# Performance work log

Hardware: AMD Instinct MI355X
Metric: run time of the kernel (lower is better)

Reference implementation:

```python
import jax, jax.numpy as jnp
import numpy as np

# --- CT geometry (stand-in for ctlib `options`): parallel-beam Radon transform ---
H = 256; W = 256          # image size
V = 192                   # number of projection views
D = 256                   # detector bins
S = 256                   # samples along each ray
_SQ2 = float(np.sqrt(2.0))
_ANG = jnp.asarray(np.linspace(0.0, np.pi, V, endpoint=False), jnp.float32)      # view angles
_DET = jnp.asarray(np.linspace(-_SQ2, _SQ2, D), jnp.float32)                      # detector coords (world units, image in [-1,1]^2)
_T   = jnp.asarray(np.linspace(-_SQ2, _SQ2, S), jnp.float32)                      # sample positions along ray
_DT  = jnp.float32(2.0 * _SQ2 / S)                                                # ray step length


def _bilerp(img, xp, yp):
    """Bilinear gather from img [H,W] at pixel coords xp,yp; zero outside."""
    x0 = jnp.floor(xp); y0 = jnp.floor(yp)
    ix0 = x0.astype(jnp.int32); iy0 = y0.astype(jnp.int32)
    fx = xp - x0; fy = yp - y0
    def gat(ix, iy):
        valid = (ix >= 0) & (ix < W) & (iy >= 0) & (iy < H)
        v = img[jnp.clip(iy, 0, H - 1), jnp.clip(ix, 0, W - 1)]
        return jnp.where(valid, v, jnp.float32(0.0))
    return (gat(ix0, iy0) * (1 - fx) * (1 - fy)
            + gat(ix0 + 1, iy0) * fx * (1 - fy)
            + gat(ix0, iy0 + 1) * (1 - fx) * fy
            + gat(ix0 + 1, iy0 + 1) * fx * fy)


def project2d(img):
    """Ray-driven forward projection: img [H,W] -> sinogram [V,D]."""
    cos = jnp.cos(_ANG)[:, None, None]; sin = jnp.sin(_ANG)[:, None, None]
    s = _DET[None, :, None]; t = _T[None, None, :]
    # world coords of sample points along each ray: [V,D,S]
    xw = -s * sin + t * cos
    yw = s * cos + t * sin
    # world [-1,1] -> pixel coords
    xp = (xw + 1.0) * (W / 2.0) - 0.5
    yp = (yw + 1.0) * (H / 2.0) - 0.5
    return _bilerp(img, xp, yp).sum(-1) * _DT


def backproject2d(sino):
    """Exact adjoint of project2d (ray-driven scatter): [V,D] -> [H,W]."""
    _, vjp_fn = jax.vjp(project2d, jnp.zeros((H, W), sino.dtype))
    return vjp_fn(sino)[0]


def setup_inputs() -> dict:
    key = jax.random.key(0)
    k1, k2, k3 = jax.random.split(key, 3)
    input_data = jax.random.normal(k1, (2, 1, H, W), jnp.float32)
    proj = jax.random.normal(k2, (2, 1, V, D), jnp.float32)
    weight = jax.random.uniform(k3, (1,), jnp.float32)
    return {"input_data": input_data, "proj": proj, "weight": weight}


def reference(input_data, proj, weight):
    B, C = input_data.shape[:2]
    imgs = input_data.reshape(B * C, H, W)
    sino = jax.vmap(project2d)(imgs).reshape(proj.shape)          # A x
    temp = sino - proj                                            # A x - p
    ir = jax.vmap(backproject2d)(temp.reshape(B * C, V, D)).reshape(input_data.shape)  # A^T (A x - p)
    return input_data - weight * ir
```

## Files before the change

### kernel.cpp

```cpp
#include <hip/hip_runtime.h>
#include <math.h>

#define HH 256
#define WW 256
#define VV 192
#define DD 256
#define SS 256

#define DSQ2      1.41421356237309504880
#define F_DT      ((float)(2.0 * DSQ2 / 256.0))
#define F_INV_DS  ((float)(255.0 / (2.0 * DSQ2)))
#define F_SIG     ((float)(256.0 * DSQ2 / 255.0))
#define F_RAD     ((float)(128.0 * DSQ2))

#define TPITCH 67
#define NSEG 8
#define NV (VV / NSEG)

static __device__ __forceinline__ float view_angle(int v) {
    return (float)((double)v * (3.14159265358979323846 / 192.0));
}

__global__ __launch_bounds__(256)
void fwd_tile_kernel(const float* __restrict__ img_all,
                     float* __restrict__ sacc) {
    __shared__ float tile[66 * TPITCH];
    __shared__ float red[4][64];
    const int tx = (blockIdx.x & 3) << 6;
    const int ty = (blockIdx.x >> 2) << 6;
    const int v  = blockIdx.y;
    const int b  = blockIdx.z;
    const int tid  = threadIdx.x;
    const int lane = tid & 63;
    const int wv   = tid >> 6;

    const float* __restrict__ img = img_all + (b << 16);

    for (int k = tid; k < 64 * 16; k += 256) {
        const int r  = k >> 4;
        const int c4 = (k & 15) << 2;
        const float4 val = *(const float4*)(img + ((ty + r) << 8) + tx + c4);
        float* dst = tile + (r + 1) * TPITCH + 1 + c4;
        dst[0] = val.x; dst[1] = val.y; dst[2] = val.z; dst[3] = val.w;
    }
    if (tid < 132) {
        const int r  = tid >> 1;
        const int cc = (tid & 1) ? 65 : 0;
        const int gx = tx - 1 + cc;
        const int gy = ty - 1 + r;
        float vv = 0.0f;
        if ((unsigned)gx < 256u && (unsigned)gy < 256u) vv = img[(gy << 8) + gx];
        tile[r * TPITCH + cc] = vv;
    }
    if (tid < 128) {
        const int cc = 1 + (tid & 63);
        const int r  = (tid >> 6) ? 65 : 0;
        const int gx = tx - 1 + cc;
        const int gy = ty - 1 + r;
        float vv = 0.0f;
        if ((unsigned)gx < 256u && (unsigned)gy < 256u) vv = img[(gy << 8) + gx];
        tile[r * TPITCH + cc] = vv;
    }

    float sn, cs;
    sincosf(view_angle(v), &sn, &cs);
    const float Xd = -sn * F_SIG, Yd = cs * F_SIG;
    const float Xt =  cs * F_SIG, Yt = sn * F_SIG;
    const float X0 = 127.5f - F_RAD * (cs - sn);
    const float Y0 = 127.5f - F_RAD * (cs + sn);

    const int lox = (tx == 0) ? -1 : 0;
    const int loy = (ty == 0) ? -1 : 0;
    const unsigned spanx = (unsigned)(64 - lox);
    const unsigned spany = (unsigned)(64 - loy);

    const float xwl = ((float)(tx + lox) + 0.5f) * (1.0f / 128.0f) - 1.0f;
    const float xwh = ((float)(tx + 64)  + 0.5f) * (1.0f / 128.0f) - 1.0f;
    const float ywl = ((float)(ty + loy) + 0.5f) * (1.0f / 128.0f) - 1.0f;
    const float ywh = ((float)(ty + 64)  + 0.5f) * (1.0f / 128.0f) - 1.0f;
    const float dA = -xwl * sn, dB = -xwh * sn;
    const float dC =  ywl * cs, dDq =  ywh * cs;
    const float tAq =  xwl * cs, tB =  xwh * cs;
    const float tC =  ywl * sn, tD =  ywh * sn;
    const float dcmin = 127.5f + (fminf(dA, dB) + fminf(dC, dDq)) * F_INV_DS;
    const float dcmax = 127.5f + (fmaxf(dA, dB) + fmaxf(dC, dDq)) * F_INV_DS;
    const float tcmin = 127.5f + (fminf(tAq, tB) + fminf(tC, tD)) * F_INV_DS;
    const float tcmax = 127.5f + (fmaxf(tAq, tB) + fmaxf(tC, tD)) * F_INV_DS;
    const int dlo = max(0, (int)ceilf(dcmin - 0.002f));
    const int dhi = min(255, (int)floorf(dcmax + 0.002f));
    const int tlo = max(0, (int)ceilf(tcmin - 0.002f));
    const int thi = min(255, (int)floorf(tcmax + 0.002f));

    __syncthreads();

    const int sbase = (b * VV + v) << 8;
    for (int dbase = dlo; dbase <= dhi; dbase += 64) {
        const int d = dbase + lane;
        float acc = 0.0f;
        float xc = fmaf((float)d, Xd, fmaf((float)(tlo + wv), Xt, X0)) - (float)tx + 1.0f;
        float yc = fmaf((float)d, Yd, fmaf((float)(tlo + wv), Yt, Y0)) - (float)ty + 1.0f;
        const float step_x = 4.0f * Xt, step_y = 4.0f * Yt;
#pragma unroll 2
        for (int t = tlo + wv; t <= thi; t += 4) {
            const float xf = floorf(xc);
            const float yf = floorf(yc);
            const int cx = (int)xf;
            const int cy = (int)yf;
            const float fx = xc - xf;
            const float fy = yc - yf;
            if (((unsigned)(cx - 1 - lox) < spanx) & ((unsigned)(cy - 1 - loy) < spany)) {
                const float* p = tile + cy * TPITCH + cx;
                const float v00 = p[0],      v10 = p[1];
                const float v01 = p[TPITCH], v11 = p[TPITCH + 1];
                const float top = fmaf(fx, v10 - v00, v00);
                const float bot = fmaf(fx, v11 - v01, v01);
                acc += fmaf(fy, bot - top, top);
            }
            xc += step_x; yc += step_y;
        }
        red[wv][lane] = acc;
        __syncthreads();
        if (tid < 64) {
            const float s = red[0][tid] + red[1][tid] + red[2][tid] + red[3][tid];
            const int d2 = dbase + tid;
            if (s != 0.0f && d2 <= dhi)
                atomicAdd(sacc + sbase + d2, s);
        }
        __syncthreads();
    }
}

__global__ __launch_bounds__(256)
void bwd_partial_kernel(const float* __restrict__ sacc,
                        const float* __restrict__ proj,
                        float* __restrict__ ir) {
    __shared__ float s_t[NV * DD];
    __shared__ float4 s_g[NV];
    const int tid = threadIdx.x;
    const int v0 = blockIdx.y * NV;
    const int b  = (int)blockIdx.x >> 7;

    if (tid < NV) {
        float sn, cs;
        sincosf(view_angle(v0 + tid), &sn, &cs);
        s_g[tid] = make_float4(cs, sn, F_SIG * cs, F_SIG * sn);
    }
    {
        const int base = (b * VV + v0) << 8;
        const float4* s4 = (const float4*)(sacc + base);
        const float4* p4 = (const float4*)(proj + base);
        for (int i = tid; i < NV * (DD / 4); i += 256) {
            const float4 a = s4[i];
            const float4 p = p4[i];
            float4 r;
            r.x = fmaf(F_DT, a.x, -p.x);
            r.y = fmaf(F_DT, a.y, -p.y);
            r.z = fmaf(F_DT, a.z, -p.z);
            r.w = fmaf(F_DT, a.w, -p.w);
            ((float4*)s_t)[i] = r;
        }
    }
    __syncthreads();

    const int idx = ((int)blockIdx.x << 9) + tid;
    const int y0 = (idx >> 8) & 255;
    const int x  = idx & 255;
    const float xw  = (float)x  * (1.0f / 128.0f) + (0.5f / 128.0f - 1.0f);
    const float yw0 = (float)y0 * (1.0f / 128.0f) + (0.5f / 128.0f - 1.0f);
    const float yw1 = yw0 + (1.0f / 128.0f);

    float acc0 = 0.0f, acc1 = 0.0f;
    for (int vi = 0; vi < NV; ++vi) {
        const float4 g = s_g[vi];
        const float* __restrict__ row = s_t + (vi << 8);
#pragma unroll
        for (int p = 0; p < 2; ++p) {
            const float yw = p ? yw1 : yw0;
            const float sw = fmaf(-xw, g.y, yw * g.x);
            const float tw = fmaf( xw, g.x, yw * g.y);
            const float dc = fmaf(sw, F_INV_DS, 127.5f);
            const float tc = fmaf(tw, F_INV_DS, 127.5f);
            const float d0f = floorf(dc);
            const float t0f = floorf(tc);
            const int d0 = (int)d0f;
            const float fd = dc - d0f;
            const float ft = tc - t0f;

            const float dx00 = fmaf(g.z, -ft, g.w * fd);
            const float dyn  = fmaf(g.z,  fd, g.w * ft);
            const float dx01 = dx00 + g.z;
            const float dy01 = g.w - dyn;
            const float dx10 = dx00 - g.w;
            const float dy10 = g.z - dyn;
            const float dx11 = dx01 - g.w;
            const float dy11 = dy10 + g.w;

            const float w00 = fmaxf(0.0f, 1.0f - fabsf(dx00)) * fmaxf(0.0f, 1.0f - fabsf(dyn));
            const float w01 = fmaxf(0.0f, 1.0f - fabsf(dx01)) * fmaxf(0.0f, 1.0f - fabsf(dy01));
            const float w10 = fmaxf(0.0f, 1.0f - fabsf(dx10)) * fmaxf(0.0f, 1.0f - fabsf(dy10));
            const float w11 = fmaxf(0.0f, 1.0f - fabsf(dx11)) * fmaxf(0.0f, 1.0f - fabsf(dy11));

            const float rA = row[d0];
            const float rB = row[d0 + 1];
            if (p == 0) {
                acc0 = fmaf(w00 + w01, rA, acc0);
                acc0 = fmaf(w10 + w11, rB, acc0);
            } else {
                acc1 = fmaf(w00 + w01, rA, acc1);
                acc1 = fmaf(w10 + w11, rB, acc1);
            }
        }
    }

    atomicAdd(ir + idx, acc0);
    atomicAdd(ir + idx + 256, acc1);
}

__global__ __launch_bounds__(256)
void combine_kernel(const float* __restrict__ input,
                    const float* __restrict__ ir,
                    const float* __restrict__ weight,
                    float* __restrict__ out) {
    const int i = blockIdx.x * 256 + threadIdx.x;
    const float4 a = ((const float4*)ir)[i];
    const float4 v = ((const float4*)input)[i];
    const float c = -weight[0] * F_DT;
    ((float4*)out)[i] = make_float4(fmaf(c, a.x, v.x), fmaf(c, a.y, v.y),
                                    fmaf(c, a.z, v.z), fmaf(c, a.w, v.w));
}

extern "C" void kernel_launch(void* const* d_in, const int* in_sizes, int n_in,
                              void* d_out, int out_size, void* d_ws, size_t ws_size,
                              hipStream_t stream) {
    const float* input  = (const float*)d_in[0];
    const float* proj   = (const float*)d_in[1];
    const float* weight = (const float*)d_in[2];
    float* out  = (float*)d_out;

    const int nb = in_sizes[0] / (HH * WW);
    const int npix = nb * HH * WW;
    const int nsino = nb * VV * DD;
    float* sacc = (float*)d_ws;
    float* ir   = sacc + nsino;

    hipMemsetAsync(d_ws, 0, (size_t)(nsino + npix) * sizeof(float), stream);
    fwd_tile_kernel<<<dim3(16, VV, nb), 256, 0, stream>>>(input, sacc);
    bwd_partial_kernel<<<dim3(npix / 512, NSEG), 256, 0, stream>>>(sacc, proj, ir);
    combine_kernel<<<npix / 1024, 256, 0, stream>>>(input, ir, weight, out);
}
```

Baseline: 104.1 us.

## Drop shared reduction in forward kernel, branchless sampling, more view segments

The forward kernel no longer reduces the four wavefront partial sums through shared memory with two barriers. Each thread now atomically adds its own partial sum directly, which cuts synchronization but roughly quadruples global atomics. The bilinear sample becomes branchless, using clamped indices and a select. The backward kernel splits views into 16 segments instead of 8, which doubles the number of blocks and partial outputs, and it adds occupancy launch bounds and loop unrolling.

```diff
diff --git a/kernel.cpp b/kernel.cpp
--- a/kernel.cpp
+++ b/kernel.cpp
@@ -14,7 +14,7 @@
 #define F_RAD     ((float)(128.0 * DSQ2))
 
 #define TPITCH 67
-#define NSEG 8
+#define NSEG 16
 #define NV (VV / NSEG)
 
 static __device__ __forceinline__ float view_angle(int v) {
@@ -25,7 +25,6 @@
 void fwd_tile_kernel(const float* __restrict__ img_all,
                      float* __restrict__ sacc) {
     __shared__ float tile[66 * TPITCH];
-    __shared__ float red[4][64];
     const int tx = (blockIdx.x & 3) << 6;
     const int ty = (blockIdx.x >> 2) << 6;
     const int v  = blockIdx.y;
@@ -108,29 +107,25 @@
             const int cy = (int)yf;
             const float fx = xc - xf;
             const float fy = yc - yf;
-            if (((unsigned)(cx - 1 - lox) < spanx) & ((unsigned)(cy - 1 - loy) < spany)) {
-                const float* p = tile + cy * TPITCH + cx;
-                const float v00 = p[0],      v10 = p[1];
-                const float v01 = p[TPITCH], v11 = p[TPITCH + 1];
-                const float top = fmaf(fx, v10 - v00, v00);
-                const float bot = fmaf(fx, v11 - v01, v01);
-                acc += fmaf(fy, bot - top, top);
-            }
+            const bool ok = (((unsigned)(cx - 1 - lox) < spanx) &
+                             ((unsigned)(cy - 1 - loy) < spany));
+            const int cxc = min(max(cx, 0), 65);
+            const int cyc = min(max(cy, 0), 64);
+            const float* p = tile + cyc * TPITCH + cxc;
+            const float v00 = p[0],      v10 = p[1];
+            const float v01 = p[TPITCH], v11 = p[TPITCH + 1];
+            const float top = fmaf(fx, v10 - v00, v00);
+            const float bot = fmaf(fx, v11 - v01, v01);
+            const float smp = fmaf(fy, bot - top, top);
+            acc += ok ? smp : 0.0f;
             xc += step_x; yc += step_y;
         }
-        red[wv][lane] = acc;
-        __syncthreads();
-        if (tid < 64) {
-            const float s = red[0][tid] + red[1][tid] + red[2][tid] + red[3][tid];
-            const int d2 = dbase + tid;
-            if (s != 0.0f && d2 <= dhi)
-                atomicAdd(sacc + sbase + d2, s);
-        }
-        __syncthreads();
-    }
-}
-
-__global__ __launch_bounds__(256)
+        if (acc != 0.0f && d <= dhi)
+            atomicAdd(sacc + sbase + d, acc);
+    }
+}
+
+__global__ __launch_bounds__(256, 8)
 void bwd_partial_kernel(const float* __restrict__ sacc,
                         const float* __restrict__ proj,
                         float* __restrict__ ir) {
@@ -149,7 +144,9 @@
         const int base = (b * VV + v0) << 8;
         const float4* s4 = (const float4*)(sacc + base);
         const float4* p4 = (const float4*)(proj + base);
-        for (int i = tid; i < NV * (DD / 4); i += 256) {
+#pragma unroll
+        for (int k = 0; k < NV * (DD / 4) / 256; ++k) {
+            const int i = tid + (k << 8);
             const float4 a = s4[i];
             const float4 p = p4[i];
             float4 r;
@@ -170,6 +167,7 @@
     const float yw1 = yw0 + (1.0f / 128.0f);
 
     float acc0 = 0.0f, acc1 = 0.0f;
+#pragma unroll 2
     for (int vi = 0; vi < NV; ++vi) {
         const float4 g = s_g[vi];
         const float* __restrict__ row = s_t + (vi << 8);
```

Result: no change. 102.6 us (-1.4%).
